# Kernel tuning notes

Hardware: AMD Instinct MI355X
Metric: run time of the kernel (lower is better)

The kernel has to match this reference:

```python
import jax, jax.numpy as jnp
import numpy as np

NUM_NODES = 100000
NUM_EDGES = 400000
F_IN = 16          # num_node_features
F_EDGE = 8         # num_edge_features
EMB = 16           # emb_size
NUM_GRAPHS = 256


def setup_inputs() -> dict:
    key = jax.random.key(0)
    ks = jax.random.split(key, 12)
    x = jax.random.normal(ks[0], (NUM_NODES, F_IN), dtype=jnp.float32)
    edge_index = jax.random.randint(ks[1], (2, NUM_EDGES), 0, NUM_NODES, dtype=jnp.int32)
    edge_attr = jax.random.normal(ks[2], (NUM_EDGES, F_EDGE), dtype=jnp.float32)
    batch = jnp.sort(jax.random.randint(ks[3], (NUM_NODES,), 0, NUM_GRAPHS, dtype=jnp.int32))
    s = 0.1
    # edge-network MLP: Linear(F_EDGE -> F_IN*EMB) + ReLU (torch Linear convention: W[out,in])
    nn1_w = jax.random.normal(ks[4], (F_IN * EMB, F_EDGE), dtype=jnp.float32) * s
    nn1_b = jax.random.normal(ks[5], (F_IN * EMB,), dtype=jnp.float32) * s
    # NNConv root weight (bias=False Linear) + separate bias
    root_w = jax.random.normal(ks[6], (EMB, F_IN), dtype=jnp.float32) * s
    conv_b = jax.random.normal(ks[7], (EMB,), dtype=jnp.float32) * s
    lin1_w = jax.random.normal(ks[8], (EMB, 2 * EMB), dtype=jnp.float32) * s
    lin1_b = jax.random.normal(ks[9], (EMB,), dtype=jnp.float32) * s
    lin2_w = jax.random.normal(ks[10], (1, EMB), dtype=jnp.float32) * s
    lin2_b = jax.random.normal(ks[11], (1,), dtype=jnp.float32) * s
    return {"x": x, "edge_index": edge_index, "edge_attr": edge_attr, "batch": batch,
            "nn1_w": nn1_w, "nn1_b": nn1_b, "root_w": root_w, "conv_b": conv_b,
            "lin1_w": lin1_w, "lin1_b": lin1_b, "lin2_w": lin2_w, "lin2_b": lin2_b}


def reference(x, edge_index, edge_attr, batch, nn1_w, nn1_b, root_w, conv_b,
              lin1_w, lin1_b, lin2_w, lin2_b):
    N = x.shape[0]
    src, dst = edge_index[0], edge_index[1]  # PyG: message flows src(j) -> dst(i)
    # edge network -> per-edge weight matrices [E, F_IN, EMB]
    w = jax.nn.relu(edge_attr @ nn1_w.T + nn1_b).reshape(-1, F_IN, EMB)
    # gather source features, per-edge matmul
    msg = jnp.einsum('ei,eio->eo', x[src], w)  # [E, EMB]
    # scatter-mean into target nodes
    sums = jax.ops.segment_sum(msg, dst, num_segments=N)
    cnt = jax.ops.segment_sum(jnp.ones((msg.shape[0],), msg.dtype), dst, num_segments=N)
    agg = sums / jnp.maximum(cnt, 1.0)[:, None]
    # NNConv: root transform + aggregated messages + bias, then outer ReLU
    h = jax.nn.relu(agg + x @ root_w.T + conv_b)  # [N, EMB]
    # global max pool and global mean pool per graph
    gmax = jax.ops.segment_max(h, batch, num_segments=NUM_GRAPHS)
    gsum = jax.ops.segment_sum(h, batch, num_segments=NUM_GRAPHS)
    gcnt = jax.ops.segment_sum(jnp.ones((N,), h.dtype), batch, num_segments=NUM_GRAPHS)
    gmean = gsum / jnp.maximum(gcnt, 1.0)[:, None]
    pooled = jnp.concatenate([gmax, gmean], axis=1)  # [G, 2*EMB]
    h2 = jax.nn.relu(pooled @ lin1_w.T + lin1_b)
    out = h2 @ lin2_w.T + lin2_b  # [G, 1]
    return out
```

## Files before the change

### kernel.cpp

```cpp
#include <hip/hip_runtime.h>

#define NUM_NODES 100000
#define NUM_EDGES 400000
#define F_IN 16
#define F_EDGE 8
#define EMB 16
#define NUM_GRAPHS 256

#define NT (NUM_EDGES / 8)
#define EDGE_GRID 2048

#define NPB 128
#define NODE_BLOCKS ((NUM_NODES + NPB - 1) / NPB)

#define WS_ZERO_FLOATS (NUM_NODES * EMB + NUM_NODES + 2 * NUM_GRAPHS * EMB + NUM_GRAPHS)

__global__ __launch_bounds__(256) void zero_kernel(float4* __restrict__ ws)
{
    const int n4 = WS_ZERO_FLOATS / 4;
    const int stride = gridDim.x * 256;
    for (int i = blockIdx.x * 256 + threadIdx.x; i < n4; i += stride)
        ws[i] = make_float4(0.f, 0.f, 0.f, 0.f);
}

__global__ __launch_bounds__(256, 3) void edge_kernel(
    const float* __restrict__ x, const int* __restrict__ ei,
    const float* __restrict__ ea, const float* __restrict__ nn1_w,
    const float* __restrict__ nn1_b, float* __restrict__ sums,
    float* __restrict__ cnt)
{
    const int tid = threadIdx.x;
    const int o   = tid & 15;
    const int ih  = (tid >> 4) & 1;
    const int eL  = tid >> 5;

    float4 w0[8], w1[8];
    float  br[8];
    #pragma unroll
    for (int ii = 0; ii < 8; ii++) {
        const int r = (ih * 8 + ii) * 16 + o;
        w0[ii] = *(const float4*)&nn1_w[r * 8];
        w1[ii] = *(const float4*)&nn1_w[r * 8 + 4];
        br[ii] = nn1_b[r];
    }

    int t = blockIdx.x;
    int e   = t * 8 + eL;
    int src = ei[e];
    int dst = ei[NUM_EDGES + e];
    float4 a0 = *(const float4*)&ea[e * 8];
    float4 a1 = *(const float4*)&ea[e * 8 + 4];
    float4 x0 = *(const float4*)&x[src * 16 + ih * 8];
    float4 x1 = *(const float4*)&x[src * 16 + ih * 8 + 4];

    while (true) {
        const int tn = t + EDGE_GRID;
        const bool more = (tn < NT);
        int srcn = 0, dstn = 0;
        float4 na0, na1, nx0, nx1;
        if (more) {
            const int en = tn * 8 + eL;
            srcn = ei[en];
            dstn = ei[NUM_EDGES + en];
            na0 = *(const float4*)&ea[en * 8];
            na1 = *(const float4*)&ea[en * 8 + 4];
            nx0 = *(const float4*)&x[srcn * 16 + ih * 8];
            nx1 = *(const float4*)&x[srcn * 16 + ih * 8 + 4];
        }

        const float xr[8] = {x0.x, x0.y, x0.z, x0.w, x1.x, x1.y, x1.z, x1.w};
        float acc = 0.f;
        #pragma unroll
        for (int ii = 0; ii < 8; ii++) {
            float u = br[ii];
            u = fmaf(a0.x, w0[ii].x, u); u = fmaf(a0.y, w0[ii].y, u);
            u = fmaf(a0.z, w0[ii].z, u); u = fmaf(a0.w, w0[ii].w, u);
            u = fmaf(a1.x, w1[ii].x, u); u = fmaf(a1.y, w1[ii].y, u);
            u = fmaf(a1.z, w1[ii].z, u); u = fmaf(a1.w, w1[ii].w, u);
            acc = fmaf(xr[ii], fmaxf(u, 0.f), acc);
        }
        acc += __shfl_xor(acc, 16);

        if (ih == 0)         atomicAdd(&sums[dst * 16 + o], acc);
        if ((tid & 31) == 0) atomicAdd(&cnt[dst], 1.f);

        if (!more) break;
        t = tn; src = srcn; dst = dstn;
        a0 = na0; a1 = na1; x0 = nx0; x1 = nx1;
    }
}

__global__ __launch_bounds__(256) void node_kernel(
    const float* __restrict__ x, const int* __restrict__ batch,
    const float* __restrict__ root_w, const float* __restrict__ conv_b,
    const float* __restrict__ sums, const float* __restrict__ cnt,
    unsigned int* __restrict__ gmax, float* __restrict__ gsum,
    float* __restrict__ gcnt)
{
    __shared__ float rwT[256];
    __shared__ float xsh[256];
    __shared__ float ssh[256];
    __shared__ float csh[16];
    __shared__ int   bsh[16];
    __shared__ float hsh[256];

    const int tid = threadIdx.x;
    const int j   = tid >> 4;
    const int o   = tid & 15;
    const int n0  = blockIdx.x * NPB;

    rwT[(tid & 15) * 16 + (tid >> 4)] = root_w[tid];
    const float cb = conv_b[o];

    int   curg = batch[n0];
    float am = 0.f, asum = 0.f, ac = 0.f;

    for (int s0 = 0; s0 < NPB; s0 += 16) {
        const int base = n0 + s0;
        const int idx  = base * 16 + tid;
        const bool v   = (idx < NUM_NODES * 16);
        const float xv = v ? x[idx]    : 0.f;
        const float sv = v ? sums[idx] : 0.f;
        float cv = 1.f; int bv = -1;
        if (tid < 16) {
            const int n = base + tid;
            if (n < NUM_NODES) { cv = cnt[n]; bv = batch[n]; }
        }
        __syncthreads();
        xsh[tid] = xv; ssh[tid] = sv;
        if (tid < 16) { csh[tid] = cv; bsh[tid] = bv; }
        __syncthreads();

        float a = cb + ssh[j * 16 + o] / fmaxf(csh[j], 1.f);
        #pragma unroll
        for (int i = 0; i < F_IN; i++)
            a = fmaf(xsh[j * 16 + i], rwT[i * 16 + o], a);
        hsh[tid] = fmaxf(a, 0.f);
        __syncthreads();

        if (tid < 16) {
            #pragma unroll 1
            for (int jj = 0; jj < 16; jj++) {
                const int g = bsh[jj];
                if (g < 0) break;
                if (g != curg) {
                    atomicMax(&gmax[curg * 16 + o], __float_as_uint(am));
                    atomicAdd(&gsum[curg * 16 + o], asum);
                    if (o == 0) atomicAdd(&gcnt[curg], ac);
                    am = 0.f; asum = 0.f; ac = 0.f; curg = g;
                }
                const float h = hsh[jj * 16 + o];
                am = fmaxf(am, h); asum += h; ac += 1.f;
            }
        }
    }

    if (tid < 16) {
        atomicMax(&gmax[curg * 16 + o], __float_as_uint(am));
        atomicAdd(&gsum[curg * 16 + o], asum);
        if (o == 0) atomicAdd(&gcnt[curg], ac);
    }
}

__global__ __launch_bounds__(256) void head_kernel(
    const unsigned int* __restrict__ gmax, const float* __restrict__ gsum,
    const float* __restrict__ gcnt,
    const float* __restrict__ lin1_w, const float* __restrict__ lin1_b,
    const float* __restrict__ lin2_w, const float* __restrict__ lin2_b,
    float* __restrict__ out)
{
    const int g = threadIdx.x;

    float pooled[2 * EMB];
    #pragma unroll
    for (int o = 0; o < EMB; o++) pooled[o] = __uint_as_float(gmax[g * 16 + o]);
    const float c = fmaxf(gcnt[g], 1.f);
    #pragma unroll
    for (int o = 0; o < EMB; o++) pooled[EMB + o] = gsum[g * 16 + o] / c;

    float acc = lin2_b[0];
    #pragma unroll
    for (int k = 0; k < EMB; k++) {
        float a = lin1_b[k];
        #pragma unroll
        for (int cc = 0; cc < 2 * EMB; cc++)
            a = fmaf(pooled[cc], lin1_w[k * 32 + cc], a);
        acc = fmaf(fmaxf(a, 0.f), lin2_w[k], acc);
    }
    out[g] = acc;
}

extern "C" void kernel_launch(void* const* d_in, const int* in_sizes, int n_in,
                              void* d_out, int out_size, void* d_ws, size_t ws_size,
                              hipStream_t stream) {
    const float* x      = (const float*)d_in[0];
    const int*   ei     = (const int*)d_in[1];
    const float* ea     = (const float*)d_in[2];
    const int*   batch  = (const int*)d_in[3];
    const float* nn1_w  = (const float*)d_in[4];
    const float* nn1_b  = (const float*)d_in[5];
    const float* root_w = (const float*)d_in[6];
    const float* conv_b = (const float*)d_in[7];
    const float* lin1_w = (const float*)d_in[8];
    const float* lin1_b = (const float*)d_in[9];
    const float* lin2_w = (const float*)d_in[10];
    const float* lin2_b = (const float*)d_in[11];
    float* out = (float*)d_out;

    float*        sums = (float*)d_ws;
    float*        cnt  = sums + (size_t)NUM_NODES * EMB;
    unsigned int* gmax = (unsigned int*)(cnt + NUM_NODES);
    float*        gsum = (float*)(gmax + NUM_GRAPHS * EMB);
    float*        gcnt = gsum + NUM_GRAPHS * EMB;

    zero_kernel<<<1024, 256, 0, stream>>>((float4*)d_ws);
    edge_kernel<<<EDGE_GRID, 256, 0, stream>>>(x, ei, ea, nn1_w, nn1_b, sums, cnt);
    node_kernel<<<NODE_BLOCKS, 256, 0, stream>>>(
        x, batch, root_w, conv_b, sums, cnt, gmax, gsum, gcnt);
    head_kernel<<<1, 256, 0, stream>>>(gmax, gsum, gcnt,
                                       lin1_w, lin1_b, lin2_w, lin2_b, out);
}
```

Baseline: 171.7 us.

## Replace atomic scatter with CSR build and fused per-node gather

Edges are bucketed by destination every call through a histogram, a three-level prefix scan and an atomic fill. A fused kernel then gathers each node's incoming edges, computes the messages, applies the mean, the root transform and the ReLU, and pools per graph, all in one pass. This removes the per-edge float atomics into a 6.4MB sums buffer and the separate node pass. In exchange it adds several small launches, integer atomics for the CSR build, and an edge order within each node that depends on atomics. Nodes with many incoming edges also leave lanes idle during the gather.

```diff
diff --git a/kernel.cpp b/kernel.cpp
--- a/kernel.cpp
+++ b/kernel.cpp
@@ -1,164 +1,184 @@
 #include <hip/hip_runtime.h>
 
-#define NUM_NODES 100000
-#define NUM_EDGES 400000
+#define NN 100000
+#define NE 400000
 #define F_IN 16
 #define F_EDGE 8
 #define EMB 16
 #define NUM_GRAPHS 256
 
-#define NT (NUM_EDGES / 8)
-#define EDGE_GRID 2048
-
-#define NPB 128
-#define NODE_BLOCKS ((NUM_NODES + NPB - 1) / NPB)
-
-#define WS_ZERO_FLOATS (NUM_NODES * EMB + NUM_NODES + 2 * NUM_GRAPHS * EMB + NUM_GRAPHS)
-
-__global__ __launch_bounds__(256) void zero_kernel(float4* __restrict__ ws)
-{
-    const int n4 = WS_ZERO_FLOATS / 4;
-    const int stride = gridDim.x * 256;
-    for (int i = blockIdx.x * 256 + threadIdx.x; i < n4; i += stride)
-        ws[i] = make_float4(0.f, 0.f, 0.f, 0.f);
-}
-
-__global__ __launch_bounds__(256, 3) void edge_kernel(
+#define NPB 64
+#define GATHER_BLOCKS ((NN + NPB - 1) / NPB)
+
+#define SCAN_BD 1024
+#define NSB ((NN + SCAN_BD - 1) / SCAN_BD)
+
+#define DEG_F4   (NN / 4)
+#define POOL_F4  ((2 * NUM_GRAPHS * EMB + NUM_GRAPHS) / 4)
+#define ZERO_F4  (DEG_F4 + POOL_F4)
+
+__global__ __launch_bounds__(256) void zero_kernel(float4* __restrict__ deg4,
+                                                   float4* __restrict__ pool4)
+{
+    const int i = blockIdx.x * 256 + threadIdx.x;
+    const float4 z = make_float4(0.f, 0.f, 0.f, 0.f);
+    if (i < DEG_F4) deg4[i] = z;
+    else if (i < ZERO_F4) pool4[i - DEG_F4] = z;
+}
+
+__global__ __launch_bounds__(256) void hist_kernel(const int* __restrict__ ei,
+                                                   int* __restrict__ deg)
+{
+    const int e = blockIdx.x * 256 + threadIdx.x;
+    if (e < NE) atomicAdd(&deg[ei[NE + e]], 1);
+}
+
+__global__ __launch_bounds__(SCAN_BD) void scan_blocks(const int* __restrict__ deg,
+                                                       int* __restrict__ rowptr,
+                                                       int* __restrict__ bsum)
+{
+    __shared__ int sh[SCAN_BD];
+    const int t = threadIdx.x;
+    const int i = blockIdx.x * SCAN_BD + t;
+    const int v = (i < NN) ? deg[i] : 0;
+    sh[t] = v;
+    __syncthreads();
+    #pragma unroll
+    for (int off = 1; off < SCAN_BD; off <<= 1) {
+        const int add = (t >= off) ? sh[t - off] : 0;
+        __syncthreads();
+        sh[t] += add;
+        __syncthreads();
+    }
+    if (i < NN) rowptr[i] = sh[t] - v;
+    if (t == SCAN_BD - 1) bsum[blockIdx.x] = sh[t];
+}
+
+__global__ __launch_bounds__(128) void scan_tops(int* __restrict__ bsum)
+{
+    __shared__ int sb[128];
+    const int t = threadIdx.x;
+    const int v = (t < NSB) ? bsum[t] : 0;
+    sb[t] = v;
+    __syncthreads();
+    #pragma unroll
+    for (int off = 1; off < 128; off <<= 1) {
+        const int add = (t >= off) ? sb[t - off] : 0;
+        __syncthreads();
+        sb[t] += add;
+        __syncthreads();
+    }
+    if (t < NSB) bsum[t] = sb[t] - v;
+}
+
+__global__ __launch_bounds__(SCAN_BD) void scan_add(int* __restrict__ rowptr,
+                                                    const int* __restrict__ bsum)
+{
+    const int i = blockIdx.x * SCAN_BD + threadIdx.x;
+    if (i < NN) rowptr[i] += bsum[blockIdx.x];
+}
+
+__global__ __launch_bounds__(256) void fill_kernel(const int* __restrict__ ei,
+                                                   int* __restrict__ rowptr,
+                                                   int* __restrict__ eid)
+{
+    const int e = blockIdx.x * 256 + threadIdx.x;
+    if (e < NE) {
+        const int dst = ei[NE + e];
+        const int pos = atomicAdd(&rowptr[dst], 1);
+        eid[pos] = e;
+    }
+}
+
+__global__ __launch_bounds__(256) void gather_node_kernel(
     const float* __restrict__ x, const int* __restrict__ ei,
     const float* __restrict__ ea, const float* __restrict__ nn1_w,
-    const float* __restrict__ nn1_b, float* __restrict__ sums,
-    float* __restrict__ cnt)
-{
+    const float* __restrict__ nn1_b, const int* __restrict__ batch,
+    const float* __restrict__ root_w, const float* __restrict__ conv_b,
+    const int* __restrict__ rowptr, const int* __restrict__ eid,
+    unsigned int* __restrict__ gmax, float* __restrict__ gsum,
+    float* __restrict__ gcnt)
+{
+    __shared__ float hsh[NPB * 16];
+    __shared__ int   bsh[NPB];
+
     const int tid = threadIdx.x;
     const int o   = tid & 15;
-    const int ih  = (tid >> 4) & 1;
-    const int eL  = tid >> 5;
-
-    float4 w0[8], w1[8];
-    float  br[8];
-    #pragma unroll
-    for (int ii = 0; ii < 8; ii++) {
-        const int r = (ih * 8 + ii) * 16 + o;
+    const int q   = (tid >> 4) & 3;
+    const int w   = tid >> 6;
+    const int n0  = blockIdx.x * NPB;
+
+    float4 w0[4], w1[4];
+    float  bb[4];
+    #pragma unroll
+    for (int ii = 0; ii < 4; ii++) {
+        const int r = (q * 4 + ii) * 16 + o;
         w0[ii] = *(const float4*)&nn1_w[r * 8];
         w1[ii] = *(const float4*)&nn1_w[r * 8 + 4];
-        br[ii] = nn1_b[r];
-    }
-
-    int t = blockIdx.x;
-    int e   = t * 8 + eL;
-    int src = ei[e];
-    int dst = ei[NUM_EDGES + e];
-    float4 a0 = *(const float4*)&ea[e * 8];
-    float4 a1 = *(const float4*)&ea[e * 8 + 4];
-    float4 x0 = *(const float4*)&x[src * 16 + ih * 8];
-    float4 x1 = *(const float4*)&x[src * 16 + ih * 8 + 4];
-
-    while (true) {
-        const int tn = t + EDGE_GRID;
-        const bool more = (tn < NT);
-        int srcn = 0, dstn = 0;
-        float4 na0, na1, nx0, nx1;
-        if (more) {
-            const int en = tn * 8 + eL;
-            srcn = ei[en];
-            dstn = ei[NUM_EDGES + en];
-            na0 = *(const float4*)&ea[en * 8];
-            na1 = *(const float4*)&ea[en * 8 + 4];
-            nx0 = *(const float4*)&x[srcn * 16 + ih * 8];
-            nx1 = *(const float4*)&x[srcn * 16 + ih * 8 + 4];
+        bb[ii] = nn1_b[r];
+    }
+    const float4 rw = *(const float4*)&root_w[o * 16 + q * 4];
+    const float  cb = conv_b[o];
+
+    if (tid < NPB) bsh[tid] = (n0 + tid < NN) ? batch[n0 + tid] : -1;
+
+    for (int k = 0; k < 16; k++) {
+        const int n = n0 + w * 16 + k;
+        if (n < NN) {
+            const int st = (n > 0) ? rowptr[n - 1] : 0;
+            const int en = rowptr[n];
+
+            float acc = 0.f;
+            for (int idx = st; idx < en; idx++) {
+                const int ev  = eid[idx];
+                const int src = ei[ev];
+                const float4 a0 = *(const float4*)&ea[ev * 8];
+                const float4 a1 = *(const float4*)&ea[ev * 8 + 4];
+                const float4 xq = *(const float4*)&x[src * 16 + q * 4];
+                const float xv[4] = {xq.x, xq.y, xq.z, xq.w};
+                #pragma unroll
+                for (int ii = 0; ii < 4; ii++) {
+                    float u = bb[ii];
+                    u = fmaf(a0.x, w0[ii].x, u); u = fmaf(a0.y, w0[ii].y, u);
+                    u = fmaf(a0.z, w0[ii].z, u); u = fmaf(a0.w, w0[ii].w, u);
+                    u = fmaf(a1.x, w1[ii].x, u); u = fmaf(a1.y, w1[ii].y, u);
+                    u = fmaf(a1.z, w1[ii].z, u); u = fmaf(a1.w, w1[ii].w, u);
+                    acc = fmaf(xv[ii], fmaxf(u, 0.f), acc);
+                }
+            }
+
+            const float4 xn = *(const float4*)&x[n * 16 + q * 4];
+            float ar = xn.x * rw.x + xn.y * rw.y + xn.z * rw.z + xn.w * rw.w;
+
+            acc += __shfl_xor(acc, 16); acc += __shfl_xor(acc, 32);
+            ar  += __shfl_xor(ar, 16);  ar  += __shfl_xor(ar, 32);
+
+            const float deg = (float)(en - st);
+            const float h = fmaxf(cb + ar + acc / fmaxf(deg, 1.f), 0.f);
+            if (q == 0) hsh[(w * 16 + k) * 16 + o] = h;
         }
-
-        const float xr[8] = {x0.x, x0.y, x0.z, x0.w, x1.x, x1.y, x1.z, x1.w};
-        float acc = 0.f;
-        #pragma unroll
-        for (int ii = 0; ii < 8; ii++) {
-            float u = br[ii];
-            u = fmaf(a0.x, w0[ii].x, u); u = fmaf(a0.y, w0[ii].y, u);
-            u = fmaf(a0.z, w0[ii].z, u); u = fmaf(a0.w, w0[ii].w, u);
-            u = fmaf(a1.x, w1[ii].x, u); u = fmaf(a1.y, w1[ii].y, u);
-            u = fmaf(a1.z, w1[ii].z, u); u = fmaf(a1.w, w1[ii].w, u);
-            acc = fmaf(xr[ii], fmaxf(u, 0.f), acc);
+    }
+    __syncthreads();
+
+    if (tid < 16) {
+        int curg = bsh[0];
+        float am = 0.f, as = 0.f, ac = 0.f;
+        #pragma unroll 1
+        for (int jj = 0; jj < NPB; jj++) {
+            const int g = bsh[jj];
+            if (g < 0) break;
+            if (g != curg) {
+                atomicMax(&gmax[curg * 16 + tid], __float_as_uint(am));
+                atomicAdd(&gsum[curg * 16 + tid], as);
+                if (tid == 0) atomicAdd(&gcnt[curg], ac);
+                am = 0.f; as = 0.f; ac = 0.f; curg = g;
+            }
+            const float h = hsh[jj * 16 + tid];
+            am = fmaxf(am, h); as += h; ac += 1.f;
         }
-        acc += __shfl_xor(acc, 16);
-
-        if (ih == 0)         atomicAdd(&sums[dst * 16 + o], acc);
-        if ((tid & 31) == 0) atomicAdd(&cnt[dst], 1.f);
-
-        if (!more) break;
-        t = tn; src = srcn; dst = dstn;
-        a0 = na0; a1 = na1; x0 = nx0; x1 = nx1;
-    }
-}
-
-__global__ __launch_bounds__(256) void node_kernel(
-    const float* __restrict__ x, const int* __restrict__ batch,
-    const float* __restrict__ root_w, const float* __restrict__ conv_b,
-    const float* __restrict__ sums, const float* __restrict__ cnt,
-    unsigned int* __restrict__ gmax, float* __restrict__ gsum,
-    float* __restrict__ gcnt)
-{
-    __shared__ float rwT[256];
-    __shared__ float xsh[256];
-    __shared__ float ssh[256];
-    __shared__ float csh[16];
-    __shared__ int   bsh[16];
-    __shared__ float hsh[256];
-
-    const int tid = threadIdx.x;
-    const int j   = tid >> 4;
-    const int o   = tid & 15;
-    const int n0  = blockIdx.x * NPB;
-
-    rwT[(tid & 15) * 16 + (tid >> 4)] = root_w[tid];
-    const float cb = conv_b[o];
-
-    int   curg = batch[n0];
-    float am = 0.f, asum = 0.f, ac = 0.f;
-
-    for (int s0 = 0; s0 < NPB; s0 += 16) {
-        const int base = n0 + s0;
-        const int idx  = base * 16 + tid;
-        const bool v   = (idx < NUM_NODES * 16);
-        const float xv = v ? x[idx]    : 0.f;
-        const float sv = v ? sums[idx] : 0.f;
-        float cv = 1.f; int bv = -1;
-        if (tid < 16) {
-            const int n = base + tid;
-            if (n < NUM_NODES) { cv = cnt[n]; bv = batch[n]; }
-        }
-        __syncthreads();
-        xsh[tid] = xv; ssh[tid] = sv;
-        if (tid < 16) { csh[tid] = cv; bsh[tid] = bv; }
-        __syncthreads();
-
-        float a = cb + ssh[j * 16 + o] / fmaxf(csh[j], 1.f);
-        #pragma unroll
-        for (int i = 0; i < F_IN; i++)
-            a = fmaf(xsh[j * 16 + i], rwT[i * 16 + o], a);
-        hsh[tid] = fmaxf(a, 0.f);
-        __syncthreads();
-
-        if (tid < 16) {
-            #pragma unroll 1
-            for (int jj = 0; jj < 16; jj++) {
-                const int g = bsh[jj];
-                if (g < 0) break;
-                if (g != curg) {
-                    atomicMax(&gmax[curg * 16 + o], __float_as_uint(am));
-                    atomicAdd(&gsum[curg * 16 + o], asum);
-                    if (o == 0) atomicAdd(&gcnt[curg], ac);
-                    am = 0.f; asum = 0.f; ac = 0.f; curg = g;
-                }
-                const float h = hsh[jj * 16 + o];
-                am = fmaxf(am, h); asum += h; ac += 1.f;
-            }
-        }
-    }
-
-    if (tid < 16) {
-        atomicMax(&gmax[curg * 16 + o], __float_as_uint(am));
-        atomicAdd(&gsum[curg * 16 + o], asum);
-        if (o == 0) atomicAdd(&gcnt[curg], ac);
+        atomicMax(&gmax[curg * 16 + tid], __float_as_uint(am));
+        atomicAdd(&gsum[curg * 16 + tid], as);
+        if (tid == 0) atomicAdd(&gcnt[curg], ac);
     }
 }
 
@@ -207,16 +227,24 @@
     const float* lin2_b = (const float*)d_in[11];
     float* out = (float*)d_out;
 
-    float*        sums = (float*)d_ws;
-    float*        cnt  = sums + (size_t)NUM_NODES * EMB;
-    unsigned int* gmax = (unsigned int*)(cnt + NUM_NODES);
-    float*        gsum = (float*)(gmax + NUM_GRAPHS * EMB);
-    float*        gcnt = gsum + NUM_GRAPHS * EMB;
-
-    zero_kernel<<<1024, 256, 0, stream>>>((float4*)d_ws);
-    edge_kernel<<<EDGE_GRID, 256, 0, stream>>>(x, ei, ea, nn1_w, nn1_b, sums, cnt);
-    node_kernel<<<NODE_BLOCKS, 256, 0, stream>>>(
-        x, batch, root_w, conv_b, sums, cnt, gmax, gsum, gcnt);
+    int*          deg    = (int*)d_ws;
+    int*          rowptr = deg + NN;
+    int*          eid    = rowptr + NN;
+    int*          bsum   = eid + NE;
+    unsigned int* gmax   = (unsigned int*)(bsum + 128);
+    float*        gsum   = (float*)(gmax + NUM_GRAPHS * EMB);
+    float*        gcnt   = gsum + NUM_GRAPHS * EMB;
+
+    zero_kernel<<<(ZERO_F4 + 255) / 256, 256, 0, stream>>>(
+        (float4*)deg, (float4*)gmax);
+    hist_kernel<<<(NE + 255) / 256, 256, 0, stream>>>(ei, deg);
+    scan_blocks<<<NSB, SCAN_BD, 0, stream>>>(deg, rowptr, bsum);
+    scan_tops<<<1, 128, 0, stream>>>(bsum);
+    scan_add<<<NSB, SCAN_BD, 0, stream>>>(rowptr, bsum);
+    fill_kernel<<<(NE + 255) / 256, 256, 0, stream>>>(ei, rowptr, eid);
+    gather_node_kernel<<<GATHER_BLOCKS, 256, 0, stream>>>(
+        x, ei, ea, nn1_w, nn1_b, batch, root_w, conv_b, rowptr, eid,
+        gmax, gsum, gcnt);
     head_kernel<<<1, 256, 0, stream>>>(gmax, gsum, gcnt,
                                        lin1_w, lin1_b, lin2_w, lin2_b, out);
 }
```

After: 271.7 us. 1.58x slower.
